# Kernel tuning notes

Hardware: AMD Instinct MI355X
Metric: run time of the kernel (lower is better)

Reference implementation:

```python
import jax, jax.numpy as jnp
import numpy as np
from jax import lax

EPS = 1e-20
DN = ('NCHW', 'OIHW', 'NCHW')


def nconv(x, c, w, b, pad):
    """Normalized convolution (Eldesokey NConv2d): conv(data*conf)/conv(conf)."""
    pads = [(pad, pad), (pad, pad)]
    denom = lax.conv_general_dilated(c, w, (1, 1), pads, dimension_numbers=DN)
    nomin = lax.conv_general_dilated(x * c, w, (1, 1), pads, dimension_numbers=DN)
    out = nomin / (denom + EPS) + b[None, :, None, None]
    s = jnp.sum(w, axis=(1, 2, 3))  # per-out-channel kernel sum
    cout = denom / s[None, :, None, None]
    return out, cout


def pool_gather(x, c):
    """2x2 stride-2 max-pool on c; gather x at the argmax locations (vectorized
    replacement for the per-(batch,channel) Python-loop unpool gather)."""
    B, C, H, W = c.shape
    cw = c.reshape(B, C, H // 2, 2, W // 2, 2).transpose(0, 1, 2, 4, 3, 5).reshape(B, C, H // 2, W // 2, 4)
    xw = x.reshape(B, C, H // 2, 2, W // 2, 2).transpose(0, 1, 2, 4, 3, 5).reshape(B, C, H // 2, W // 2, 4)
    idx = jnp.argmax(cw, axis=-1)[..., None]
    c_ds = jnp.take_along_axis(cw, idx, axis=-1)[..., 0]
    x_ds = jnp.take_along_axis(xw, idx, axis=-1)[..., 0]
    return x_ds, c_ds / 4.0


def up2(a):
    """Nearest-neighbor 2x upsample (exact-doubling case of F.interpolate)."""
    return jnp.repeat(jnp.repeat(a, 2, axis=2), 2, axis=3)


def setup_inputs() -> dict:
    key = jax.random.key(0)
    ks = jax.random.split(key, 16)
    C = 32  # (input_channels-1) * mid_channels = 1 * 32
    u = lambda k, sh: jax.random.uniform(k, sh, dtype=jnp.float32) * 0.05
    z = lambda k, sh: jax.random.normal(k, sh, dtype=jnp.float32) * 0.01
    return {
        'x': jax.random.uniform(ks[0], (2, 2, 512, 512), dtype=jnp.float32),
        'w1': u(ks[1], (C, 1, 5, 5)), 'b1': z(ks[2], (C,)),
        'w2': u(ks[3], (C, C, 5, 5)), 'b2': z(ks[4], (C,)),
        'w3': u(ks[5], (C, C, 5, 5)), 'b3': z(ks[6], (C,)),
        'w4': u(ks[7], (C, 2 * C, 3, 3)), 'b4': z(ks[8], (C,)),
        'w5': u(ks[9], (C, 2 * C, 3, 3)), 'b5': z(ks[10], (C,)),
        'w6': u(ks[11], (C, 2 * C, 3, 3)), 'b6': z(ks[12], (C,)),
        'w7': u(ks[13], (1, C, 1, 1)), 'b7': z(ks[14], (1,)),
    }


def reference(x, w1, b1, w2, b2, w3, b3, w4, b4, w5, b5, w6, b6, w7, b7):
    cat = lambda a, b: jnp.concatenate((a, b), axis=1)
    x0 = x[:, 0:1]                                 # data channel
    c0 = jnp.broadcast_to(x[:, 1:2], x0.shape)     # confidence channel repeated
    x1, c1 = nconv(x0, c0, w1, b1, 2)
    x1, c1 = nconv(x1, c1, w2, b2, 2)
    x1, c1 = nconv(x1, c1, w3, b3, 2)
    x1_ds, c1_ds = pool_gather(x1, c1)
    x2_ds, c2_ds = nconv(x1_ds, c1_ds, w2, b2, 2)  # nconv2 weight reuse (as in source)
    x2_ds, c2_ds = nconv(x2_ds, c2_ds, w3, b3, 2)
    x2_dss, c2_dss = pool_gather(x2_ds, c2_ds)
    x3_ds, c3_ds = nconv(x2_dss, c2_dss, w2, b2, 2)
    x3_dss, c3_dss = pool_gather(x3_ds, c3_ds)
    x4_ds, c4_ds = nconv(x3_dss, c3_dss, w2, b2, 2)
    x4, c4 = up2(x4_ds), up2(c4_ds)
    x34_ds, c34_ds = nconv(cat(x3_ds, x4), cat(c3_ds, c4), w4, b4, 1)
    x34, c34 = up2(x34_ds), up2(c34_ds)
    x23_ds, c23_ds = nconv(cat(x2_ds, x34), cat(c2_ds, c34), w5, b5, 1)
    x23, c23 = up2(x23_ds), up2(c23_ds)
    xout, cout = nconv(cat(x23, x1), cat(c23, c1), w6, b6, 1)
    xout, cout = nconv(xout, cout, w7, b7, 0)
    return xout
```

## Files before the change

### kernel.cpp

```cpp
#include <hip/hip_runtime.h>
#include <hip/hip_bf16.h>

#define EPSF 1e-20f

using short8  = __attribute__((ext_vector_type(8))) short;
using float4f = __attribute__((ext_vector_type(4))) float;
typedef const __attribute__((address_space(1))) unsigned int* gas_t;
typedef __attribute__((address_space(3))) unsigned int* las_t;

__device__ __forceinline__ unsigned short f2bf(float f) {
    __hip_bfloat16 h = __float2bfloat16(f);
    return __builtin_bit_cast(unsigned short, h);
}
__device__ __forceinline__ float bf2f(unsigned short u) {
    __hip_bfloat16 h = __builtin_bit_cast(__hip_bfloat16, u);
    return __bfloat162float(h);
}
__device__ __forceinline__ float frcp(float x) { return __builtin_amdgcn_rcpf(x); }

__global__ void wprep_k(const float* __restrict__ w1, const float* __restrict__ w2,
                        const float* __restrict__ w3, const float* __restrict__ w4,
                        const float* __restrict__ w5, const float* __restrict__ w6,
                        float* __restrict__ wt1,
                        float* __restrict__ is1, float* __restrict__ is2,
                        float* __restrict__ is3, float* __restrict__ is4,
                        float* __restrict__ is5, float* __restrict__ is6,
                        unsigned short* __restrict__ wf2, unsigned short* __restrict__ wf3,
                        unsigned short* __restrict__ wf4, unsigned short* __restrict__ wf5,
                        unsigned short* __restrict__ wf6,
                        unsigned int* __restrict__ zpage) {
    const int tid = threadIdx.x;
    if (blockIdx.x == 0 && tid < 4) zpage[tid] = 0;
    if (blockIdx.x >= 420) {
        int wid = (blockIdx.x - 420) * 4 + (tid >> 6);
        if (wid >= 192) return;
        int task = wid >> 5, co = wid & 31, lane = tid & 63;
        const float* w; int n; float* s;
        switch (task) {
            case 0: w = w1; n = 25;  s = is1; break;
            case 1: w = w2; n = 800; s = is2; break;
            case 2: w = w3; n = 800; s = is3; break;
            case 3: w = w4; n = 576; s = is4; break;
            case 4: w = w5; n = 576; s = is5; break;
            default: w = w6; n = 576; s = is6; break;
        }
        float acc = 0.f;
        for (int i = lane; i < n; i += 64) acc += w[co * n + i];
#pragma unroll
        for (int off = 1; off < 64; off <<= 1) acc += __shfl_xor(acc, off);
        if (lane == 0) s[co] = 1.0f / acc;
        return;
    }
    int idx = blockIdx.x * 256 + tid;
    if (idx < 800) {
        int co = idx / 25, t = idx % 25;
        wt1[t * 32 + co] = w1[idx];
        return;
    }
    if (idx < 992) return;
    int r = idx - 992;
    const float* w; unsigned short* wf; int CIN, KK, cxor;
    if (r < 25600)        {             w = w2; wf = wf2; CIN = 32; KK = 25; cxor = 0;  }
    else if (r < 51200)   { r -= 25600; w = w3; wf = wf3; CIN = 32; KK = 25; cxor = 0;  }
    else if (r < 69632)   { r -= 51200; w = w4; wf = wf4; CIN = 64; KK = 9;  cxor = 0;  }
    else if (r < 88064)   { r -= 69632; w = w5; wf = wf5; CIN = 64; KK = 9;  cxor = 0;  }
    else if (r < 106496)  { r -= 88064; w = w6; wf = wf6; CIN = 64; KK = 9;  cxor = 32; }
    else return;
    int j = r & 7, lane = (r >> 3) & 63, cot = (r >> 9) & 1, ks = r >> 10;
    int phase = ks / KK, tap = ks - phase * KK;
    int co = cot * 16 + (lane & 15);
    int ci = (phase * 32 + (lane >> 4) * 8 + j) ^ cxor;
    wf[r] = f2bf(w[((long)co * CIN + ci) * KK + tap]);
}

__global__ __launch_bounds__(256)
void conv1_k(const float* __restrict__ x, const float* __restrict__ wt,
             const float* __restrict__ bias, const float* __restrict__ is_,
             unsigned short* __restrict__ out, int H, int W) {
    constexpr int TIW = 36, TIH = 12, TSZ = TIW * TIH;
    __shared__ float sc[TSZ], sp[TSZ];
    const int tid = threadIdx.x;
    const int tx = tid & 31, ty = tid >> 5;
    const int ox0 = blockIdx.x * 32, oy0 = blockIdx.y * 8, b = blockIdx.z;
    const long HW = (long)H * W;
    const float* xd = x + (long)(b * 2) * HW;
    const float* xc = xd + HW;

    for (int i = tid; i < TSZ; i += 256) {
        int py = i / TIW, px = i - py * TIW;
        int gy = oy0 - 2 + py, gx = ox0 - 2 + px;
        float c = 0.f, d = 0.f;
        if (gy >= 0 && gy < H && gx >= 0 && gx < W) {
            long g = (long)gy * W + gx;
            c = xc[g]; d = xd[g];
        }
        sc[i] = c;
        sp[i] = d * c;
    }
    __syncthreads();

    float ac[32], ap[32];
#pragma unroll
    for (int i = 0; i < 32; ++i) { ac[i] = 0.f; ap[i] = 0.f; }
#pragma unroll
    for (int dy = 0; dy < 5; ++dy) {
#pragma unroll
        for (int dx = 0; dx < 5; ++dx) {
            const int li = (ty + dy) * TIW + tx + dx;
            float cf = sc[li];
            float pv = sp[li];
            const float* wr = wt + (dy * 5 + dx) * 32;
#pragma unroll
            for (int co = 0; co < 32; ++co) {
                ac[co] = fmaf(wr[co], cf, ac[co]);
                ap[co] = fmaf(wr[co], pv, ap[co]);
            }
        }
    }

    const int xx = ox0 + tx, yy = oy0 + ty;
    unsigned short* po = out + ((long)(b * 2 + 0) * HW + (long)yy * W + xx) * 32;
    unsigned short* co_ = out + ((long)(b * 2 + 1) * HW + (long)yy * W + xx) * 32;
#pragma unroll
    for (int g = 0; g < 4; ++g) {
        uint4 vp, vc;
        unsigned int pw[4], cw[4];
#pragma unroll
        for (int h = 0; h < 4; ++h) {
            int c0 = g * 8 + h * 2, c1 = c0 + 1;
            float d0 = ac[c0], d1 = ac[c1];
            float ox0v = fmaf(ap[c0], frcp(d0 + EPSF), bias[c0]);
            float ox1v = fmaf(ap[c1], frcp(d1 + EPSF), bias[c1]);
            float oc0 = d0 * is_[c0], oc1 = d1 * is_[c1];
            pw[h] = (unsigned int)f2bf(ox0v * oc0) | ((unsigned int)f2bf(ox1v * oc1) << 16);
            cw[h] = (unsigned int)f2bf(oc0) | ((unsigned int)f2bf(oc1) << 16);
        }
        vp.x = pw[0]; vp.y = pw[1]; vp.z = pw[2]; vp.w = pw[3];
        vc.x = cw[0]; vc.y = cw[1]; vc.z = cw[2]; vc.w = cw[3];
        *(uint4*)(po + g * 8) = vp;
        *(uint4*)(co_ + g * 8) = vc;
    }
}

template <int KS, int NPH, bool FUSE7, bool POOL>
__global__ __launch_bounds__(256, 4)
void mconv_k(const unsigned short* __restrict__ s1,
             const unsigned short* __restrict__ s2,
             const unsigned short* __restrict__ wf,
             const float* __restrict__ bias, const float* __restrict__ sden,
             unsigned short* __restrict__ out, float* __restrict__ xout,
             const float* __restrict__ w7, const float* __restrict__ b7,
             unsigned short* __restrict__ pout,
             const unsigned int* __restrict__ zpage,
             int H, int W) {
    constexpr int R = KS / 2, KK = KS * KS;
    constexpr int TIH = 8 + KS - 1, TIW = 16 + KS - 1;
    constexpr int PCS = TIH * TIW * 32;
    constexpr int NCH = TIH * TIW * 4;
    __shared__ unsigned short lds[2 * PCS];

    const int tid = threadIdx.x;
    const int wv = tid >> 6, lane = tid & 63, n = lane & 15, q = lane >> 4;
    const int ox0 = blockIdx.x * 16, oy0 = blockIdx.y * 8, b = blockIdx.z;
    const long HW = (long)H * W;

    float4f accP[2][2], accC[2][2];
#pragma unroll
    for (int mt = 0; mt < 2; ++mt)
#pragma unroll
        for (int ct = 0; ct < 2; ++ct) {
            accP[mt][ct] = (float4f)0.f;
            accC[mt][ct] = (float4f)0.f;
        }

    const int PB = (2 * wv) * TIW + n;

    for (int ph = 0; ph < NPH; ++ph) {
        const unsigned short* src = (NPH == 2 && ph == 1) ? s2 : s1;
        if (ph) __syncthreads();
        for (int it = 0; it < (2 * NCH + 255) / 256; ++it) {
            int ch = it * 256 + tid;
            if (ch < 2 * NCH) {
                int pc = ch / NCH, c2 = ch - pc * NCH;
                int pix = c2 >> 2, k8 = c2 & 3;
                int py = pix / TIW, px = pix - py * TIW;
                int gy = oy0 - R + py, gx = ox0 - R + px;
                const unsigned short* ga;
                if (gy >= 0 && gy < H && gx >= 0 && gx < W) {
                    long gi;
                    if (NPH == 2 && ph == 1)
                        gi = ((long)(b * 2 + pc) * (HW >> 2) +
                              (long)(gy >> 1) * (W >> 1) + (gx >> 1)) * 32 + k8 * 8;
                    else
                        gi = ((long)(b * 2 + pc) * HW + (long)gy * W + gx) * 32 + k8 * 8;
                    ga = src + gi;
                } else {
                    ga = (const unsigned short*)zpage;
                }
                __builtin_amdgcn_global_load_lds(
                    (gas_t)ga,
                    (las_t)(lds + (size_t)(it * 256 + wv * 64) * 8),
                    16, 0, 0);
            }
        }
        __syncthreads();
#pragma unroll
        for (int dx = 0; dx < KS; ++dx) {
            short8 a0p, a1p;
#pragma unroll
            for (int r = 0; r < KS + 1; ++r) {
                short8 a0c, a1c;
                if (r < KS) {
                    const int ks = ph * KK + r * KS + dx;
                    a0c = ((const short8*)wf)[(ks * 2 + 0) * 64 + lane];
                    a1c = ((const short8*)wf)[(ks * 2 + 1) * 64 + lane];
                }
                const int p = PB + r * TIW + dx;
                const int off = p * 32 + q * 8;
                short8 bp = *(const short8*)(lds + off);
                short8 bc = *(const short8*)(lds + off + PCS);
                if (r < KS) {
                    accP[0][0] = __builtin_amdgcn_mfma_f32_16x16x32_bf16(a0c, bp, accP[0][0], 0, 0, 0);
                    accP[0][1] = __builtin_amdgcn_mfma_f32_16x16x32_bf16(a1c, bp, accP[0][1], 0, 0, 0);
                    accC[0][0] = __builtin_amdgcn_mfma_f32_16x16x32_bf16(a0c, bc, accC[0][0], 0, 0, 0);
                    accC[0][1] = __builtin_amdgcn_mfma_f32_16x16x32_bf16(a1c, bc, accC[0][1], 0, 0, 0);
                }
                if (r >= 1) {
                    accP[1][0] = __builtin_amdgcn_mfma_f32_16x16x32_bf16(a0p, bp, accP[1][0], 0, 0, 0);
                    accP[1][1] = __builtin_amdgcn_mfma_f32_16x16x32_bf16(a1p, bp, accP[1][1], 0, 0, 0);
                    accC[1][0] = __builtin_amdgcn_mfma_f32_16x16x32_bf16(a0p, bc, accC[1][0], 0, 0, 0);
                    accC[1][1] = __builtin_amdgcn_mfma_f32_16x16x32_bf16(a1p, bc, accC[1][1], 0, 0, 0);
                }
                a0p = a0c; a1p = a1c;
            }
        }
    }

    float4f b4[2], s4[2];
    b4[0] = *(const float4f*)(bias + q * 4);
    b4[1] = *(const float4f*)(bias + 16 + q * 4);
    s4[0] = *(const float4f*)(sden + q * 4);
    s4[1] = *(const float4f*)(sden + 16 + q * 4);

    if (!FUSE7) {
        if (POOL) {
            const int W2 = W >> 1;
            const long HW4 = HW >> 2;
#pragma unroll
            for (int ct = 0; ct < 2; ++ct) {
                unsigned int pw[2], cw[2];
                unsigned short ps[4], cs[4];
#pragma unroll
                for (int r = 0; r < 4; ++r) {
                    float d0 = accC[0][ct][r], d1 = accC[1][ct][r];
                    float c00 = d0 * s4[ct][r];
                    float c10 = d1 * s4[ct][r];
                    float p00 = fmaf(accP[0][ct][r], frcp(d0 + EPSF), b4[ct][r]) * c00;
                    float p10 = fmaf(accP[1][ct][r], frcp(d1 + EPSF), b4[ct][r]) * c10;
                    float c01 = __shfl_xor(c00, 1), c11 = __shfl_xor(c10, 1);
                    float p01 = __shfl_xor(p00, 1), p11 = __shfl_xor(p10, 1);
                    float bc = c00, bp = p00;
                    if (c01 > bc) { bc = c01; bp = p01; }
                    if (c10 > bc) { bc = c10; bp = p10; }
                    if (c11 > bc) { bc = c11; bp = p11; }
                    ps[r] = f2bf(bp * 0.25f);
                    cs[r] = f2bf(bc * 0.25f);
                }
                if (!(n & 1)) {
                    pw[0] = (unsigned int)ps[0] | ((unsigned int)ps[1] << 16);
                    pw[1] = (unsigned int)ps[2] | ((unsigned int)ps[3] << 16);
                    cw[0] = (unsigned int)cs[0] | ((unsigned int)cs[1] << 16);
                    cw[1] = (unsigned int)cs[2] | ((unsigned int)cs[3] << 16);
                    int gy2 = (oy0 >> 1) + wv, gx2 = (ox0 >> 1) + (n >> 1);
                    long pb = ((long)gy2 * W2 + gx2) * 32 + ct * 16 + q * 4;
                    uint2 vp; vp.x = pw[0]; vp.y = pw[1];
                    uint2 vc; vc.x = cw[0]; vc.y = cw[1];
                    *(uint2*)(pout + (long)(b * 2 + 0) * HW4 * 32 + pb) = vp;
                    *(uint2*)(pout + (long)(b * 2 + 1) * HW4 * 32 + pb) = vc;
                }
            }
        }
#pragma unroll
        for (int pl = 0; pl < 2; ++pl) {
            __syncthreads();
#pragma unroll
            for (int mt = 0; mt < 2; ++mt) {
                const int pix = (2 * wv + mt) * 16 + n;
#pragma unroll
                for (int ct = 0; ct < 2; ++ct) {
                    unsigned int w0, w1;
                    if (pl == 0) {
                        float d0 = accC[mt][ct][0], d1 = accC[mt][ct][1];
                        float d2 = accC[mt][ct][2], d3 = accC[mt][ct][3];
                        float x0 = fmaf(accP[mt][ct][0], frcp(d0 + EPSF), b4[ct][0]) * (d0 * s4[ct][0]);
                        float x1 = fmaf(accP[mt][ct][1], frcp(d1 + EPSF), b4[ct][1]) * (d1 * s4[ct][1]);
                        float x2 = fmaf(accP[mt][ct][2], frcp(d2 + EPSF), b4[ct][2]) * (d2 * s4[ct][2]);
                        float x3 = fmaf(accP[mt][ct][3], frcp(d3 + EPSF), b4[ct][3]) * (d3 * s4[ct][3]);
                        w0 = (unsigned int)f2bf(x0) | ((unsigned int)f2bf(x1) << 16);
                        w1 = (unsigned int)f2bf(x2) | ((unsigned int)f2bf(x3) << 16);
                    } else {
                        float c0 = accC[mt][ct][0] * s4[ct][0], c1 = accC[mt][ct][1] * s4[ct][1];
                        float c2 = accC[mt][ct][2] * s4[ct][2], c3 = accC[mt][ct][3] * s4[ct][3];
                        w0 = (unsigned int)f2bf(c0) | ((unsigned int)f2bf(c1) << 16);
                        w1 = (unsigned int)f2bf(c2) | ((unsigned int)f2bf(c3) << 16);
                    }
                    uint2 v; v.x = w0; v.y = w1;
                    *(uint2*)(lds + pix * 32 +
                              ((ct * 2 + (q >> 1) + n + (n >> 2)) & 3) * 8 + (q & 1) * 4) = v;
                }
            }
            __syncthreads();
            const unsigned short* obase = out + (long)(b * 2 + pl) * HW * 32;
#pragma unroll
            for (int it = 0; it < 2; ++it) {
                int off = it * 256 + tid;
                int pix = off >> 2, sub = off & 3;
                uint4 v = *(const uint4*)(lds + pix * 32 + ((sub + pix + (pix >> 2)) & 3) * 8);
                int ry = pix >> 4, rx = pix & 15;
                *(uint4*)(obase + ((long)(oy0 + ry) * W + ox0 + rx) * 32 + sub * 8) = v;
            }
        }
    } else {
        float4f w74[2];
        w74[0] = *(const float4f*)(w7 + q * 4);
        w74[1] = *(const float4f*)(w7 + 16 + q * 4);
        const float b7v = b7[0];
#pragma unroll
        for (int mt = 0; mt < 2; ++mt) {
            float num = 0.f, den = 0.f;
#pragma unroll
            for (int ct = 0; ct < 2; ++ct)
#pragma unroll
                for (int r = 0; r < 4; ++r) {
                    float d = accC[mt][ct][r];
                    float oxv = fmaf(accP[mt][ct][r], frcp(d + EPSF), b4[ct][r]);
                    float oc = d * s4[ct][r];
                    num = fmaf(w74[ct][r], oxv * oc, num);
                    den = fmaf(w74[ct][r], oc, den);
                }
            num += __shfl_xor(num, 16); num += __shfl_xor(num, 32);
            den += __shfl_xor(den, 16); den += __shfl_xor(den, 32);
            if (q == 0) {
                const int oy = oy0 + 2 * wv + mt;
                const int ox = ox0 + n;
                xout[(long)b * HW + (long)oy * W + ox] = fmaf(num, frcp(den + EPSF), b7v);
            }
        }
    }
}

extern "C" void kernel_launch(void* const* d_in, const int* in_sizes, int n_in,
                              void* d_out, int out_size, void* d_ws, size_t ws_size,
                              hipStream_t stream) {
    const float* x  = (const float*)d_in[0];
    const float* w1 = (const float*)d_in[1];
    const float* b1 = (const float*)d_in[2];
    const float* w2 = (const float*)d_in[3];
    const float* b2 = (const float*)d_in[4];
    const float* w3 = (const float*)d_in[5];
    const float* b3 = (const float*)d_in[6];
    const float* w4 = (const float*)d_in[7];
    const float* b4 = (const float*)d_in[8];
    const float* w5 = (const float*)d_in[9];
    const float* b5 = (const float*)d_in[10];
    const float* w6 = (const float*)d_in[11];
    const float* b6 = (const float*)d_in[12];
    const float* w7 = (const float*)d_in[13];
    const float* b7 = (const float*)d_in[14];

    const size_t HW1 = 512 * 512, HW2s = 256 * 256, HW3s = 128 * 128, HW4s = 64 * 64;

    const size_t WARENA = 400000;
    float* fa = (float*)d_ws;
    float *wt1 = fa;
    float *s1 = wt1 + 800, *s2 = s1 + 32, *s3 = s2 + 32;
    float *s4 = s3 + 32, *s5 = s4 + 32, *s6 = s5 + 32;
    unsigned int* zpage = (unsigned int*)(fa + 992);
    unsigned short* ua = (unsigned short*)((char*)d_ws + 4096);
    unsigned short *wf2 = ua;
    unsigned short *wf3 = wf2 + 25600;
    unsigned short *wf4 = wf3 + 25600;
    unsigned short *wf5 = wf4 + 18432;
    unsigned short *wf6 = wf5 + 18432;
    unsigned short* buf = (unsigned short*)((char*)d_ws + WARENA);

    const size_t E1 = 2 * 2 * HW1 * 32;
    const size_t E2 = 2 * 2 * HW2s * 32, E3 = 2 * 2 * HW3s * 32, E4 = 2 * 2 * HW4s * 32;
    unsigned short* A = buf;
    unsigned short* B = A + E1;
    unsigned short* P = B;
    unsigned short* Q = P + E2;
    unsigned short* S = Q + E2;
    unsigned short* T = S + E3;
    unsigned short* U = T + E3;
    unsigned short* V = U + E4;

    if (ws_size < WARENA + 2 * E1 * sizeof(unsigned short)) return;

    wprep_k<<<468, 256, 0, stream>>>(w1, w2, w3, w4, w5, w6,
                                     wt1, s1, s2, s3, s4, s5, s6,
                                     wf2, wf3, wf4, wf5, wf6, zpage);

    dim3 blkm(256);
    dim3 g1c(16, 64, 2);
    dim3 g1(32, 64, 2), g2(16, 32, 2), g3(8, 16, 2), g4(4, 8, 2);

    conv1_k<<<g1c, blkm, 0, stream>>>(x, wt1, b1, s1, A, 512, 512);
    mconv_k<5, 1, false, false><<<g1, blkm, 0, stream>>>(A, nullptr, wf2, b2, s2, B, nullptr, nullptr, nullptr, nullptr, zpage, 512, 512);
    mconv_k<5, 1, false, true><<<g1, blkm, 0, stream>>>(B, nullptr, wf3, b3, s3, A, nullptr, nullptr, nullptr, P, zpage, 512, 512);

    mconv_k<5, 1, false, false><<<g2, blkm, 0, stream>>>(P, nullptr, wf2, b2, s2, Q, nullptr, nullptr, nullptr, nullptr, zpage, 256, 256);
    mconv_k<5, 1, false, true><<<g2, blkm, 0, stream>>>(Q, nullptr, wf3, b3, s3, P, nullptr, nullptr, nullptr, S, zpage, 256, 256);

    mconv_k<5, 1, false, true><<<g3, blkm, 0, stream>>>(S, nullptr, wf2, b2, s2, T, nullptr, nullptr, nullptr, U, zpage, 128, 128);

    mconv_k<5, 1, false, false><<<g4, blkm, 0, stream>>>(U, nullptr, wf2, b2, s2, V, nullptr, nullptr, nullptr, nullptr, zpage, 64, 64);

    mconv_k<3, 2, false, false><<<g3, blkm, 0, stream>>>(T, V, wf4, b4, s4, S, nullptr, nullptr, nullptr, nullptr, zpage, 128, 128);
    mconv_k<3, 2, false, false><<<g2, blkm, 0, stream>>>(P, S, wf5, b5, s5, Q, nullptr, nullptr, nullptr, nullptr, zpage, 256, 256);
    mconv_k<3, 2, true, false><<<g1, blkm, 0, stream>>>(A, Q, wf6, b6, s6, nullptr, (float*)d_out, w7, b7, nullptr, zpage, 512, 512);
}
```

Baseline: 371.9 us.

## Rewrite first normalized conv on bf16 MFMA with LDS-staged coalesced stores

The first 1-to-32 channel 5x5 normalized convolution now runs as bf16 16x16x32 MFMA operations instead of scalar fp32 FMAs. The 25 taps are padded to 32 and the prepacked weights are stored in a new bf16 fragment layout. Outputs are staged through a swizzled LDS buffer so each plane is written with coalesced 16-byte stores. Tiles shrink to 16x8, and inputs and weights are rounded to bf16, which loses some precision on the first layer.

```diff
diff --git a/kernel.cpp b/kernel.cpp
--- a/kernel.cpp
+++ b/kernel.cpp
@@ -21,18 +21,17 @@
 __global__ void wprep_k(const float* __restrict__ w1, const float* __restrict__ w2,
                         const float* __restrict__ w3, const float* __restrict__ w4,
                         const float* __restrict__ w5, const float* __restrict__ w6,
-                        float* __restrict__ wt1,
                         float* __restrict__ is1, float* __restrict__ is2,
                         float* __restrict__ is3, float* __restrict__ is4,
                         float* __restrict__ is5, float* __restrict__ is6,
                         unsigned short* __restrict__ wf2, unsigned short* __restrict__ wf3,
                         unsigned short* __restrict__ wf4, unsigned short* __restrict__ wf5,
-                        unsigned short* __restrict__ wf6,
+                        unsigned short* __restrict__ wf6, unsigned short* __restrict__ wf1,
                         unsigned int* __restrict__ zpage) {
     const int tid = threadIdx.x;
     if (blockIdx.x == 0 && tid < 4) zpage[tid] = 0;
-    if (blockIdx.x >= 420) {
-        int wid = (blockIdx.x - 420) * 4 + (tid >> 6);
+    if (blockIdx.x >= 424) {
+        int wid = (blockIdx.x - 424) * 4 + (tid >> 6);
         if (wid >= 192) return;
         int task = wid >> 5, co = wid & 31, lane = tid & 63;
         const float* w; int n; float* s;
@@ -52,20 +51,23 @@
         return;
     }
     int idx = blockIdx.x * 256 + tid;
-    if (idx < 800) {
-        int co = idx / 25, t = idx % 25;
-        wt1[t * 32 + co] = w1[idx];
-        return;
-    }
     if (idx < 992) return;
     int r = idx - 992;
+    if (r >= 106496) {
+        int r2 = r - 106496;
+        if (r2 >= 1024) return;
+        int j = r2 & 7, lane = (r2 >> 3) & 63, cot = (r2 >> 9) & 1;
+        int co = cot * 16 + (lane & 15);
+        int tap = (lane >> 4) * 8 + j;
+        wf1[r2] = f2bf(tap < 25 ? w1[co * 25 + tap] : 0.f);
+        return;
+    }
     const float* w; unsigned short* wf; int CIN, KK, cxor;
     if (r < 25600)        {             w = w2; wf = wf2; CIN = 32; KK = 25; cxor = 0;  }
     else if (r < 51200)   { r -= 25600; w = w3; wf = wf3; CIN = 32; KK = 25; cxor = 0;  }
     else if (r < 69632)   { r -= 51200; w = w4; wf = wf4; CIN = 64; KK = 9;  cxor = 0;  }
     else if (r < 88064)   { r -= 69632; w = w5; wf = wf5; CIN = 64; KK = 9;  cxor = 0;  }
-    else if (r < 106496)  { r -= 88064; w = w6; wf = wf6; CIN = 64; KK = 9;  cxor = 32; }
-    else return;
+    else                  { r -= 88064; w = w6; wf = wf6; CIN = 64; KK = 9;  cxor = 32; }
     int j = r & 7, lane = (r >> 3) & 63, cot = (r >> 9) & 1, ks = r >> 10;
     int phase = ks / KK, tap = ks - phase * KK;
     int co = cot * 16 + (lane & 15);
@@ -74,14 +76,15 @@
 }
 
 __global__ __launch_bounds__(256)
-void conv1_k(const float* __restrict__ x, const float* __restrict__ wt,
+void conv1_k(const float* __restrict__ x, const unsigned short* __restrict__ wf1,
              const float* __restrict__ bias, const float* __restrict__ is_,
              unsigned short* __restrict__ out, int H, int W) {
-    constexpr int TIW = 36, TIH = 12, TSZ = TIW * TIH;
-    __shared__ float sc[TSZ], sp[TSZ];
+    constexpr int TIW = 20, TIH = 14, TSZ = TIW * TIH;
+    __shared__ unsigned short sp[TSZ], sc_[TSZ];
+    __shared__ unsigned short lbb[128 * 32];
     const int tid = threadIdx.x;
-    const int tx = tid & 31, ty = tid >> 5;
-    const int ox0 = blockIdx.x * 32, oy0 = blockIdx.y * 8, b = blockIdx.z;
+    const int wv = tid >> 6, lane = tid & 63, n = lane & 15, q = lane >> 4;
+    const int ox0 = blockIdx.x * 16, oy0 = blockIdx.y * 8, b = blockIdx.z;
     const long HW = (long)H * W;
     const float* xd = x + (long)(b * 2) * HW;
     const float* xc = xd + HW;
@@ -94,51 +97,82 @@
             long g = (long)gy * W + gx;
             c = xc[g]; d = xd[g];
         }
-        sc[i] = c;
-        sp[i] = d * c;
+        sc_[i] = f2bf(c);
+        sp[i] = f2bf(d * c);
     }
     __syncthreads();
 
-    float ac[32], ap[32];
-#pragma unroll
-    for (int i = 0; i < 32; ++i) { ac[i] = 0.f; ap[i] = 0.f; }
-#pragma unroll
-    for (int dy = 0; dy < 5; ++dy) {
-#pragma unroll
-        for (int dx = 0; dx < 5; ++dx) {
-            const int li = (ty + dy) * TIW + tx + dx;
-            float cf = sc[li];
-            float pv = sp[li];
-            const float* wr = wt + (dy * 5 + dx) * 32;
-#pragma unroll
-            for (int co = 0; co < 32; ++co) {
-                ac[co] = fmaf(wr[co], cf, ac[co]);
-                ap[co] = fmaf(wr[co], pv, ap[co]);
-            }
-        }
-    }
-
-    const int xx = ox0 + tx, yy = oy0 + ty;
-    unsigned short* po = out + ((long)(b * 2 + 0) * HW + (long)yy * W + xx) * 32;
-    unsigned short* co_ = out + ((long)(b * 2 + 1) * HW + (long)yy * W + xx) * 32;
-#pragma unroll
-    for (int g = 0; g < 4; ++g) {
-        uint4 vp, vc;
-        unsigned int pw[4], cw[4];
-#pragma unroll
-        for (int h = 0; h < 4; ++h) {
-            int c0 = g * 8 + h * 2, c1 = c0 + 1;
-            float d0 = ac[c0], d1 = ac[c1];
-            float ox0v = fmaf(ap[c0], frcp(d0 + EPSF), bias[c0]);
-            float ox1v = fmaf(ap[c1], frcp(d1 + EPSF), bias[c1]);
-            float oc0 = d0 * is_[c0], oc1 = d1 * is_[c1];
-            pw[h] = (unsigned int)f2bf(ox0v * oc0) | ((unsigned int)f2bf(ox1v * oc1) << 16);
-            cw[h] = (unsigned int)f2bf(oc0) | ((unsigned int)f2bf(oc1) << 16);
-        }
-        vp.x = pw[0]; vp.y = pw[1]; vp.z = pw[2]; vp.w = pw[3];
-        vc.x = cw[0]; vc.y = cw[1]; vc.z = cw[2]; vc.w = cw[3];
-        *(uint4*)(po + g * 8) = vp;
-        *(uint4*)(co_ + g * 8) = vc;
+    int loff[8];
+#pragma unroll
+    for (int j = 0; j < 8; ++j) {
+        int k = q * 8 + j;
+        int dy = k / 5, dx = k - 5 * dy;
+        loff[j] = dy * TIW + dx;
+    }
+    short8 a0 = ((const short8*)wf1)[0 * 64 + lane];
+    short8 a1 = ((const short8*)wf1)[1 * 64 + lane];
+
+    float4f accP[2][2], accC[2][2];
+#pragma unroll
+    for (int mt = 0; mt < 2; ++mt) {
+        const int rb = (2 * wv + mt) * TIW + n;
+        union { short8 v; unsigned short s[8]; } bp, bc;
+#pragma unroll
+        for (int j = 0; j < 8; ++j) {
+            bp.s[j] = sp[rb + loff[j]];
+            bc.s[j] = sc_[rb + loff[j]];
+        }
+        accP[mt][0] = __builtin_amdgcn_mfma_f32_16x16x32_bf16(a0, bp.v, (float4f)0.f, 0, 0, 0);
+        accP[mt][1] = __builtin_amdgcn_mfma_f32_16x16x32_bf16(a1, bp.v, (float4f)0.f, 0, 0, 0);
+        accC[mt][0] = __builtin_amdgcn_mfma_f32_16x16x32_bf16(a0, bc.v, (float4f)0.f, 0, 0, 0);
+        accC[mt][1] = __builtin_amdgcn_mfma_f32_16x16x32_bf16(a1, bc.v, (float4f)0.f, 0, 0, 0);
+    }
+
+    float4f b4[2], s4[2];
+    b4[0] = *(const float4f*)(bias + q * 4);
+    b4[1] = *(const float4f*)(bias + 16 + q * 4);
+    s4[0] = *(const float4f*)(is_ + q * 4);
+    s4[1] = *(const float4f*)(is_ + 16 + q * 4);
+
+#pragma unroll
+    for (int pl = 0; pl < 2; ++pl) {
+        __syncthreads();
+#pragma unroll
+        for (int mt = 0; mt < 2; ++mt) {
+            const int pix = (2 * wv + mt) * 16 + n;
+#pragma unroll
+            for (int ct = 0; ct < 2; ++ct) {
+                unsigned int w0, w1v;
+                if (pl == 0) {
+                    float d0 = accC[mt][ct][0], d1 = accC[mt][ct][1];
+                    float d2 = accC[mt][ct][2], d3 = accC[mt][ct][3];
+                    float x0 = fmaf(accP[mt][ct][0], frcp(d0 + EPSF), b4[ct][0]) * (d0 * s4[ct][0]);
+                    float x1 = fmaf(accP[mt][ct][1], frcp(d1 + EPSF), b4[ct][1]) * (d1 * s4[ct][1]);
+                    float x2 = fmaf(accP[mt][ct][2], frcp(d2 + EPSF), b4[ct][2]) * (d2 * s4[ct][2]);
+                    float x3 = fmaf(accP[mt][ct][3], frcp(d3 + EPSF), b4[ct][3]) * (d3 * s4[ct][3]);
+                    w0 = (unsigned int)f2bf(x0) | ((unsigned int)f2bf(x1) << 16);
+                    w1v = (unsigned int)f2bf(x2) | ((unsigned int)f2bf(x3) << 16);
+                } else {
+                    float c0 = accC[mt][ct][0] * s4[ct][0], c1 = accC[mt][ct][1] * s4[ct][1];
+                    float c2 = accC[mt][ct][2] * s4[ct][2], c3 = accC[mt][ct][3] * s4[ct][3];
+                    w0 = (unsigned int)f2bf(c0) | ((unsigned int)f2bf(c1) << 16);
+                    w1v = (unsigned int)f2bf(c2) | ((unsigned int)f2bf(c3) << 16);
+                }
+                uint2 v; v.x = w0; v.y = w1v;
+                *(uint2*)(lbb + pix * 32 +
+                          ((ct * 2 + (q >> 1) + n + (n >> 2)) & 3) * 8 + (q & 1) * 4) = v;
+            }
+        }
+        __syncthreads();
+        const unsigned short* obase = out + (long)(b * 2 + pl) * HW * 32;
+#pragma unroll
+        for (int it = 0; it < 2; ++it) {
+            int off = it * 256 + tid;
+            int pix = off >> 2, sub = off & 3;
+            uint4 v = *(const uint4*)(lbb + pix * 32 + ((sub + pix + (pix >> 2)) & 3) * 8);
+            int ry = pix >> 4, rx = pix & 15;
+            *(uint4*)(obase + ((long)(oy0 + ry) * W + ox0 + rx) * 32 + sub * 8) = v;
+        }
     }
 }
 
@@ -372,16 +406,16 @@
 
     const size_t WARENA = 400000;
     float* fa = (float*)d_ws;
-    float *wt1 = fa;
-    float *s1 = wt1 + 800, *s2 = s1 + 32, *s3 = s2 + 32;
+    float *s1 = fa, *s2 = s1 + 32, *s3 = s2 + 32;
     float *s4 = s3 + 32, *s5 = s4 + 32, *s6 = s5 + 32;
-    unsigned int* zpage = (unsigned int*)(fa + 992);
+    unsigned int* zpage = (unsigned int*)(fa + 192);
     unsigned short* ua = (unsigned short*)((char*)d_ws + 4096);
     unsigned short *wf2 = ua;
     unsigned short *wf3 = wf2 + 25600;
     unsigned short *wf4 = wf3 + 25600;
     unsigned short *wf5 = wf4 + 18432;
     unsigned short *wf6 = wf5 + 18432;
+    unsigned short *wf1 = wf6 + 18432;
     unsigned short* buf = (unsigned short*)((char*)d_ws + WARENA);
 
     const size_t E1 = 2 * 2 * HW1 * 32;
@@ -397,15 +431,14 @@
 
     if (ws_size < WARENA + 2 * E1 * sizeof(unsigned short)) return;
 
-    wprep_k<<<468, 256, 0, stream>>>(w1, w2, w3, w4, w5, w6,
-                                     wt1, s1, s2, s3, s4, s5, s6,
-                                     wf2, wf3, wf4, wf5, wf6, zpage);
+    wprep_k<<<472, 256, 0, stream>>>(w1, w2, w3, w4, w5, w6,
+                                     s1, s2, s3, s4, s5, s6,
+                                     wf2, wf3, wf4, wf5, wf6, wf1, zpage);
 
     dim3 blkm(256);
-    dim3 g1c(16, 64, 2);
     dim3 g1(32, 64, 2), g2(16, 32, 2), g3(8, 16, 2), g4(4, 8, 2);
 
-    conv1_k<<<g1c, blkm, 0, stream>>>(x, wt1, b1, s1, A, 512, 512);
+    conv1_k<<<g1, blkm, 0, stream>>>(x, wf1, b1, s1, A, 512, 512);
     mconv_k<5, 1, false, false><<<g1, blkm, 0, stream>>>(A, nullptr, wf2, b2, s2, B, nullptr, nullptr, nullptr, nullptr, zpage, 512, 512);
     mconv_k<5, 1, false, true><<<g1, blkm, 0, stream>>>(B, nullptr, wf3, b3, s3, A, nullptr, nullptr, nullptr, P, zpage, 512, 512);
 
```

Measured after the change: 325.2 us. -12.6%, faster.
